# Optimization experiments

Hardware: AMD Instinct MI355X
Metric: run time of the kernel (lower is better)

The kernel has to match this reference:

```python
import jax, jax.numpy as jnp
import numpy as np
from jax import lax


def _conv_layer(x, K, k, stride, pad):
    """Faithful reimplementation of the custom Conv2d, including its two quirks:
    1) weight/input flatten-order mismatch: K.reshape(k*k*cin, cout) pairs flat
       index m (decoded as kh,kw,cin for K) against x flattened as (cin,kh,kw),
       so the effective conv weight is K.reshape(-1,cout).reshape(cin,k,k,cout).
    2) the python loop range(0, padd-k, stride) misses the last valid position
       whenever (padd-k) is divisible by stride, leaving last row/col zero.
    """
    B, cin, s_in, _ = x.shape
    cout = K.shape[-1]
    out_size = (s_in + 2 * pad - k) // stride + 1
    padd = s_in + 2 * pad
    n_loop = -(-(padd - k) // stride)  # = len(range(0, padd-k, stride))
    xp = jnp.pad(x, ((0, 0), (0, 0), (pad, pad), (pad, pad))) if pad > 0 else x
    # effective weight honoring the flatten-order mismatch: (cin, kh, kw, cout)
    W = K.reshape(-1, cout).reshape(cin, k, k, cout)
    y = lax.conv_general_dilated(
        xp, W, window_strides=(stride, stride), padding='VALID',
        dimension_numbers=('NCHW', 'IHWO', 'NCHW'))
    n = min(n_loop, out_size)
    out = jnp.zeros((B, cout, out_size, out_size), x.dtype)
    out = out.at[:, :, :n, :n].set(y[:, :, :n, :n])
    return out


def setup_inputs() -> dict:
    key = jax.random.key(0)
    ks = jax.random.split(key, 9)
    NUM_CLASSES = 10
    B = 8192

    def kinit(k_, shape):
        fan_in = shape[1] * int(np.prod(shape[2:]))  # torch fan_in for 4D
        bound = float(np.sqrt(6.0 / fan_in))
        return jax.random.uniform(k_, shape, jnp.float32, -bound, bound)

    x = jax.random.normal(ks[0], (B, 3, 28, 28), jnp.float32)
    K1 = kinit(ks[1], (5, 5, 3, 8))
    K2 = kinit(ks[2], (3, 3, 8, 16))
    K3 = kinit(ks[3], (3, 3, 16, 16))
    K4 = kinit(ks[4], (3, 3, 16, 16))
    K5 = kinit(ks[5], (3, 3, 16, 16))
    K6 = kinit(ks[6], (5, 5, 16, 32))
    fc_in = 6 * 6 * 32  # 1152
    bw = float(np.sqrt(1.0 / fc_in))
    Wfc = jax.random.uniform(ks[7], (NUM_CLASSES, fc_in), jnp.float32, -bw, bw)
    bfc = jax.random.uniform(ks[8], (NUM_CLASSES,), jnp.float32, -bw, bw)
    return {"x": x, "K1": K1, "K2": K2, "K3": K3, "K4": K4, "K5": K5,
            "K6": K6, "Wfc": Wfc, "bfc": bfc}


def reference(x, K1, K2, K3, K4, K5, K6, Wfc, bfc):
    h = jax.nn.relu(_conv_layer(x, K1, 5, 2, 1))   # (B,8,13,13)
    h = jax.nn.relu(_conv_layer(h, K2, 3, 1, 1))   # (B,16,13,13), last row/col zero
    h = jax.nn.relu(_conv_layer(h, K3, 3, 1, 1))
    h = jax.nn.relu(_conv_layer(h, K4, 3, 1, 1))
    h = jax.nn.relu(_conv_layer(h, K5, 3, 1, 1))
    h = _conv_layer(h, K6, 5, 2, 1)                # (B,32,6,6), last row/col zero
    flat = h.reshape(h.shape[0], -1)               # (B,1152)
    logits = flat @ Wfc.T + bfc
    return jax.nn.softmax(logits, axis=1)
```

## Files before the change

kernel.cpp:

```cpp
#include <hip/hip_runtime.h>
#include <hip/hip_bf16.h>
#include <math.h>

#define TPB 320

typedef __attribute__((ext_vector_type(8))) short short8;
typedef __attribute__((ext_vector_type(4))) float f32x4;
typedef unsigned short u16;

__device__ __forceinline__ f32x4 MFMA(short8 a, short8 b, f32x4 c) {
    return __builtin_amdgcn_mfma_f32_16x16x32_bf16(a, b, c, 0, 0, 0);
}
__device__ __forceinline__ u16 f2bf(float f) {
    unsigned int u = __builtin_bit_cast(unsigned int, f);
    u += 0x7FFFu + ((u >> 16) & 1u);
    return (u16)(u >> 16);
}
__device__ __forceinline__ u16 f2bf_hw(float f) {
    __hip_bfloat16 b = __float2bfloat16(f);
    return __builtin_bit_cast(u16, b);
}
__device__ __forceinline__ float bf2f(u16 h) {
    unsigned int u = ((unsigned int)h) << 16;
    return __builtin_bit_cast(float, u);
}

extern "C" __global__ void prep_w(const float* __restrict__ K1, const float* __restrict__ K2,
                                  const float* __restrict__ K3, const float* __restrict__ K4,
                                  const float* __restrict__ K5, const float* __restrict__ K6,
                                  short8* __restrict__ W)
{
    const int slot = blockIdx.x * blockDim.x + threadIdx.x;
    if (slot >= 6144) return;
    const int lane = slot & 63;
    const int ent  = slot >> 6;
    const int o    = lane & 15;
    const int lhi  = lane >> 4;
    float w[8];
    int hl;
    if (ent < 6) {
        const int s = ent >> 1; hl = ent & 1;
        const int t = s * 4 + lhi;
#pragma unroll
        for (int j = 0; j < 8; j++)
            w[j] = (t < 9) ? K2[(j * 9 + t) * 16 + o] : 0.f;
    } else if (ent < 36) {
        const int e  = ent - 6;
        const float* Kg = (e < 10) ? K3 : (e < 20) ? K4 : K5;
        const int el = e % 10;
        const int s  = el >> 1; hl = el & 1;
        const int chalf = (lhi & 1) * 8;
        const int t = 2 * s + (lhi >> 1);
#pragma unroll
        for (int j = 0; j < 8; j++)
            w[j] = (t < 9) ? Kg[((chalf + j) * 9 + t) * 16 + o] : 0.f;
    } else if (ent < 88) {
        const int e = ent - 36;
        const int s = e >> 2; hl = (e >> 1) & 1;
        const int nh = e & 1;
        const int chalf = (lhi & 1) * 8;
        const int t  = 2 * s + (lhi >> 1);
        const int oo = nh * 16 + o;
#pragma unroll
        for (int j = 0; j < 8; j++)
            w[j] = (t < 25) ? K6[((chalf + j) * 25 + t) * 32 + oo] : 0.f;
    } else {
        const int e = ent - 88;
        const int s = e >> 1; hl = e & 1;
        const int g  = s * 4 + lhi;
        const int gc = g > 14 ? 14 : g;
        const int c  = (gc * 52) >> 8;
        const int kh = gc - 5 * c;
#pragma unroll
        for (int j = 0; j < 8; j++)
            w[j] = (g < 15 && o < 8 && j < 5) ? K1[(c * 25 + kh * 5 + j) * 8 + o] : 0.f;
    }
    short8 v;
#pragma unroll
    for (int j = 0; j < 8; j++) {
        const u16 h = f2bf(w[j]);
        v[j] = hl ? (short)f2bf(w[j] - bf2f(h)) : (short)h;
    }
    W[slot] = v;
}


__device__ __forceinline__ void conv8(const u16* __restrict__ s0,
                                      u16* __restrict__ d0,
                                      const short8* __restrict__ Wt,
                                      int wave, int lane, int rot)
{
    const int o   = lane & 15;
    const int lhi = lane >> 4;
    short8 Bhi[3], Blo[3];
#pragma unroll
    for (int s = 0; s < 3; s++) {
        Bhi[s] = Wt[(s * 2 + 0) * 64 + lane];
        Blo[s] = Wt[(s * 2 + 1) * 64 + lane];
    }
    const u16* sl = s0 + 3600;
    const int r0 = lane & 15;

    auto tile = [&](int m) {
        const int p  = m * 16 + r0;
        const int ip = (p * 683) >> 13;
        const int jp = p - 12 * ip;
        f32x4 acc = {0.f, 0.f, 0.f, 0.f};
#pragma unroll
        for (int s = 0; s < 3; s++) {
            const int t  = s * 4 + lhi;
            const int tt = t > 8 ? 8 : t;
            const int kh = (tt * 11) >> 5;
            const int kw = tt - 3 * kh;
            const int px = (ip + kh) * 15 + (jp + kw);
            const short8 Ahi = *(const short8*)(s0 + px * 8);
            const short8 Alo = *(const short8*)(sl + px * 8);
            acc = MFMA(Ahi, Bhi[s], acc);
            acc = MFMA(Alo, Bhi[s], acc);
            acc = MFMA(Ahi, Blo[s], acc);
        }
        const int p0 = m * 16 + lhi * 4;
#pragma unroll
        for (int r = 0; r < 4; r++) {
            const int pp = p0 + r;
            const int ii = (pp * 683) >> 13;
            const int jj = pp - 12 * ii;
            const float v = fmaxf(acc[r], 0.f);
            const u16 h = f2bf_hw(v);
            const int px2 = (ii + 1) * 15 + (jj + 1);
            const int da  = (o >> 3) * 1800 + px2 * 8 + (o & 7);
            d0[da]        = h;
            d0[da + 3600] = f2bf_hw(v - bf2f(h));
        }
    };
    int m0 = wave + rot;
    if (m0 >= 5) m0 -= 5;
    tile(m0);
    if (m0 <= 3) tile(m0 + 5);
}

__device__ __forceinline__ void conv16(const u16* __restrict__ s0,
                                       u16* __restrict__ d0,
                                       const short8* __restrict__ Wt,
                                       int wave, int lane, int rot)
{
    const int o    = lane & 15;
    const int lhi  = lane >> 4;
    const int hsel = lhi & 1;
    const int tsel = lhi >> 1;
    short8 Bhi[5], Blo[5];
#pragma unroll
    for (int s = 0; s < 5; s++) {
        Bhi[s] = Wt[(s * 2 + 0) * 64 + lane];
        Blo[s] = Wt[(s * 2 + 1) * 64 + lane];
    }
    const u16* sh = s0 + hsel * 1800;
    const u16* sl = sh + 3600;
    const int r0 = lane & 15;

    auto tile = [&](int m) {
        const int p  = m * 16 + r0;
        const int ip = (p * 683) >> 13;
        const int jp = p - 12 * ip;
        f32x4 acc = {0.f, 0.f, 0.f, 0.f};
#pragma unroll
        for (int s = 0; s < 5; s++) {
            const int t  = 2 * s + tsel;
            const int tt = t > 8 ? 8 : t;
            const int kh = (tt * 11) >> 5;
            const int kw = tt - 3 * kh;
            const int px = (ip + kh) * 15 + (jp + kw);
            const short8 Ahi = *(const short8*)(sh + px * 8);
            const short8 Alo = *(const short8*)(sl + px * 8);
            acc = MFMA(Ahi, Bhi[s], acc);
            acc = MFMA(Alo, Bhi[s], acc);
            acc = MFMA(Ahi, Blo[s], acc);
        }
        const int p0 = m * 16 + lhi * 4;
#pragma unroll
        for (int r = 0; r < 4; r++) {
            const int pp = p0 + r;
            const int ii = (pp * 683) >> 13;
            const int jj = pp - 12 * ii;
            const float v = fmaxf(acc[r], 0.f);
            const u16 h = f2bf_hw(v);
            const int px2 = (ii + 1) * 15 + (jj + 1);
            const int da  = (o >> 3) * 1800 + px2 * 8 + (o & 7);
            d0[da]        = h;
            d0[da + 3600] = f2bf_hw(v - bf2f(h));
        }
    };
    int m0 = wave + rot;
    if (m0 >= 5) m0 -= 5;
    tile(m0);
    if (m0 <= 3) tile(m0 + 5);
}

extern "C" __global__ void __launch_bounds__(TPB)
cnn_fused(const float* __restrict__ xg,
          const float* __restrict__ Wfc, const float* __restrict__ bfc,
          const short8* __restrict__ W, float* __restrict__ out)
{
    __shared__ __align__(16) unsigned char smem[28864];
    u16*   const Ah   = (u16*)smem;
    u16*   const Bh   = (u16*)(smem + 14400);
    u16*   const Sh   = (u16*)(smem + 14400);
    float* const sF   = (float*)(smem + 14400);
    float* const sLog = (float*)(smem + 28800);
    uint4* const z4   = (uint4*)smem;
    const uint4 Z = {0u, 0u, 0u, 0u};

    const int tid  = threadIdx.x;
    const int lane = tid & 63;
    const int wave = tid >> 6;
    const int img  = blockIdx.x;

    for (int i = tid; i < 1804; i += TPB) z4[i] = Z;
    __syncthreads();

    const float4* xi4 = (const float4*)(xg + (size_t)img * 2352);
    for (int i4 = tid; i4 < 588; i4 += TPB) {
        const float4 v = xi4[i4];
        const int c = i4 / 196;
        const int rem = i4 - c * 196;
        const int r = rem / 7;
        const int q = rem - r * 7;
        const int ad = c * 960 + (r + 1) * 32 + q * 4 + 1;
        const float vv[4] = {v.x, v.y, v.z, v.w};
#pragma unroll
        for (int e = 0; e < 4; e++) {
            const u16 h = f2bf_hw(vv[e]);
            Sh[ad + e]        = h;
            Sh[ad + e + 2880] = f2bf_hw(vv[e] - bf2f(h));
        }
    }
    __syncthreads();

    {
        const short8* Wt1 = W + 5632;
        const int o   = lane & 15;
        const int lhi = lane >> 4;
        short8 B1h[4], B1l[4];
#pragma unroll
        for (int s = 0; s < 4; s++) {
            B1h[s] = Wt1[(s * 2 + 0) * 64 + lane];
            B1l[s] = Wt1[(s * 2 + 1) * 64 + lane];
        }
        const u16* slo = Sh + 2880;
        for (int m = wave; m < 11; m += 5) {
            const int p  = m * 16 + o;
            const int pc = p > 168 ? 168 : p;
            const int i = (pc * 316) >> 12;
            const int j = pc - 13 * i;
            f32x4 acc = {0.f, 0.f, 0.f, 0.f};
#pragma unroll
            for (int s = 0; s < 4; s++) {
                const int g  = s * 4 + lhi;
                const int gc = g > 14 ? 14 : g;
                const int c  = (gc * 52) >> 8;
                const int kh = gc - 5 * c;
                const int ad = c * 960 + (2 * i + kh) * 32 + 2 * j;
                const short8 Ahi = *(const short8*)(Sh + ad);
                const short8 Alo = *(const short8*)(slo + ad);
                acc = MFMA(Ahi, B1h[s], acc);
                acc = MFMA(Alo, B1h[s], acc);
                acc = MFMA(Ahi, B1l[s], acc);
            }
#pragma unroll
            for (int r = 0; r < 4; r++) {
                const int pp = m * 16 + lhi * 4 + r;
                if (pp < 169 && o < 8) {
                    const int ii = (pp * 316) >> 12;
                    const int jj = pp - 13 * ii;
                    const float v = fmaxf(acc[r], 0.f);
                    const u16 h = f2bf_hw(v);
                    const int da = ((ii + 1) * 15 + (jj + 1)) * 8 + o;
                    Ah[da]        = h;
                    Ah[da + 3600] = f2bf_hw(v - bf2f(h));
                }
            }
        }
    }
    __syncthreads();

    conv8(Ah, Bh, W, wave, lane, 0);
    if (tid < 208) {
        const int pl = tid / 52, e = tid - pl * 52;
        const int px = (e < 14) ? e
                     : (e < 28) ? 195 + (e - 14)
                     : (e < 40) ? (e - 27) * 15
                                : (e - 39) * 15 + 13;
        z4[900 + pl * 225 + px] = Z;
    }
    __syncthreads();

    conv16(Bh, Ah, W + 384, wave, lane, 1);
    if (tid < 108) {
        const int pl = tid / 27, e = tid - pl * 27;
        const int px = (e < 14) ? 195 + e : (e - 14) * 15 + 13;
        z4[pl * 225 + px] = Z;
    }
    __syncthreads();

    conv16(Ah, Bh, W + 1024, wave, lane, 2);
    __syncthreads();
    conv16(Bh, Ah, W + 1664, wave, lane, 3);
    __syncthreads();

    for (int i = tid; i < 352; i += TPB) {
        const int o = i / 11, k = i - o * 11;
        const int slot = (k < 6) ? o * 36 + 30 + k : o * 36 + (k - 6) * 6 + 5;
        sF[slot] = 0.f;
    }
    if (wave < 4) {
        const short8* Wt6 = W + 2304;
        const int mt   = wave >> 1;
        const int nh   = wave & 1;
        const int lhi  = lane >> 4;
        const int hsel = lhi & 1;
        const int tsel = lhi >> 1;
        const int o    = nh * 16 + (lane & 15);
        const int pr = mt * 16 + (lane & 15);
        const int pe = pr < 25 ? pr : 0;
        const int ia = (pe * 52) >> 8;
        const int ja = pe - 5 * ia;
        const u16* sh = Ah + hsel * 1800;
        const u16* sl = sh + 3600;
        f32x4 acc = {0.f, 0.f, 0.f, 0.f};
#pragma unroll 4
        for (int s = 0; s < 13; s++) {
            const int t  = 2 * s + tsel;
            const int tt = t > 24 ? 24 : t;
            const int kh = (tt * 52) >> 8;
            const int kw = tt - 5 * kh;
            const int px = (2 * ia + kh) * 15 + (2 * ja + kw);
            const short8 Ahi = *(const short8*)(sh + px * 8);
            const short8 Alo = *(const short8*)(sl + px * 8);
            const short8 Bh2 = Wt6[((s * 2 + 0) * 2 + nh) * 64 + lane];
            const short8 Bl2 = Wt6[((s * 2 + 1) * 2 + nh) * 64 + lane];
            acc = MFMA(Ahi, Bh2, acc);
            acc = MFMA(Alo, Bh2, acc);
            acc = MFMA(Ahi, Bl2, acc);
        }
        const int p0 = mt * 16 + lhi * 4;
#pragma unroll
        for (int r = 0; r < 4; r++) {
            const int pp = p0 + r;
            if (pp < 25) {
                const int ii = (pp * 52) >> 8;
                const int jj = pp - 5 * ii;
                sF[o * 36 + ii * 6 + jj] = acc[r];
            }
        }
    }
    __syncthreads();

    if (tid < 160) {
        const int c = tid >> 4;
        const int l = tid & 15;
        const float4* fv = (const float4*)(sF + l * 72);
        const float4* wv = (const float4*)(Wfc + c * 1152 + l * 72);
        float p = 0.f;
#pragma unroll
        for (int m = 0; m < 18; m++) {
            const float4 a = fv[m];
            const float4 b = wv[m];
            p = fmaf(a.x, b.x, p);
            p = fmaf(a.y, b.y, p);
            p = fmaf(a.z, b.z, p);
            p = fmaf(a.w, b.w, p);
        }
        p += __shfl_down(p, 8, 16);
        p += __shfl_down(p, 4, 16);
        p += __shfl_down(p, 2, 16);
        p += __shfl_down(p, 1, 16);
        if (l == 0) sLog[c] = p + bfc[c];
    }
    __syncthreads();

    if (tid < 10) {
        float mx = sLog[0];
#pragma unroll
        for (int k = 1; k < 10; k++) mx = fmaxf(mx, sLog[k]);
        float s = 0.f;
#pragma unroll
        for (int k = 0; k < 10; k++) s += expf(sLog[k] - mx);
        out[(size_t)img * 10 + tid] = expf(sLog[tid] - mx) / s;
    }
}

extern "C" void kernel_launch(void* const* d_in, const int* in_sizes, int n_in,
                              void* d_out, int out_size, void* d_ws, size_t ws_size,
                              hipStream_t stream) {
    const float* x   = (const float*)d_in[0];
    const float* K1  = (const float*)d_in[1];
    const float* K2  = (const float*)d_in[2];
    const float* K3  = (const float*)d_in[3];
    const float* K4  = (const float*)d_in[4];
    const float* K5  = (const float*)d_in[5];
    const float* K6  = (const float*)d_in[6];
    const float* Wfc = (const float*)d_in[7];
    const float* bfc = (const float*)d_in[8];
    float* out = (float*)d_out;
    short8* W = (short8*)d_ws;

    prep_w<<<24, 256, 0, stream>>>(K1, K2, K3, K4, K5, K6, W);

    const int B = in_sizes[0] / 2352;
    cnn_fused<<<B, TPB, 0, stream>>>(x, Wfc, bfc, W, out);
}
```

Baseline: 251.9 us.

## Use four waves per block and split MFMA accumulators into two chains

Reduces the block from five to four waves and redistributes the 9 (or 11) M-tiles of each conv stage across four waves, with wave 0 taking an extra tile. Each MFMA sequence now accumulates into two independent accumulators (hi*hi vs correction terms), summed at the end, which shortens the dependent MFMA chain. Fewer threads per block could allow more resident blocks, but the work is less evenly balanced across waves and register use rises. Other stages that use tid thresholds (e.g. tid<208, tid<160) still fit within 256 threads.

```diff
diff --git a/kernel.cpp b/kernel.cpp
--- a/kernel.cpp
+++ b/kernel.cpp
@@ -2,7 +2,7 @@
 #include <hip/hip_bf16.h>
 #include <math.h>
 
-#define TPB 320
+#define TPB 256
 
 typedef __attribute__((ext_vector_type(8))) short short8;
 typedef __attribute__((ext_vector_type(4))) float f32x4;
@@ -105,7 +105,8 @@
         const int p  = m * 16 + r0;
         const int ip = (p * 683) >> 13;
         const int jp = p - 12 * ip;
-        f32x4 acc = {0.f, 0.f, 0.f, 0.f};
+        f32x4 accA = {0.f, 0.f, 0.f, 0.f};
+        f32x4 accB = {0.f, 0.f, 0.f, 0.f};
 #pragma unroll
         for (int s = 0; s < 3; s++) {
             const int t  = s * 4 + lhi;
@@ -115,9 +116,9 @@
             const int px = (ip + kh) * 15 + (jp + kw);
             const short8 Ahi = *(const short8*)(s0 + px * 8);
             const short8 Alo = *(const short8*)(sl + px * 8);
-            acc = MFMA(Ahi, Bhi[s], acc);
-            acc = MFMA(Alo, Bhi[s], acc);
-            acc = MFMA(Ahi, Blo[s], acc);
+            accA = MFMA(Ahi, Bhi[s], accA);
+            accB = MFMA(Alo, Bhi[s], accB);
+            accB = MFMA(Ahi, Blo[s], accB);
         }
         const int p0 = m * 16 + lhi * 4;
 #pragma unroll
@@ -125,7 +126,7 @@
             const int pp = p0 + r;
             const int ii = (pp * 683) >> 13;
             const int jj = pp - 12 * ii;
-            const float v = fmaxf(acc[r], 0.f);
+            const float v = fmaxf(accA[r] + accB[r], 0.f);
             const u16 h = f2bf_hw(v);
             const int px2 = (ii + 1) * 15 + (jj + 1);
             const int da  = (o >> 3) * 1800 + px2 * 8 + (o & 7);
@@ -133,10 +134,10 @@
             d0[da + 3600] = f2bf_hw(v - bf2f(h));
         }
     };
-    int m0 = wave + rot;
-    if (m0 >= 5) m0 -= 5;
+    const int m0 = (wave + rot) & 3;
     tile(m0);
-    if (m0 <= 3) tile(m0 + 5);
+    tile(m0 + 4);
+    if (m0 == 0) tile(8);
 }
 
 __device__ __forceinline__ void conv16(const u16* __restrict__ s0,
@@ -162,7 +163,8 @@
         const int p  = m * 16 + r0;
         const int ip = (p * 683) >> 13;
         const int jp = p - 12 * ip;
-        f32x4 acc = {0.f, 0.f, 0.f, 0.f};
+        f32x4 accA = {0.f, 0.f, 0.f, 0.f};
+        f32x4 accB = {0.f, 0.f, 0.f, 0.f};
 #pragma unroll
         for (int s = 0; s < 5; s++) {
             const int t  = 2 * s + tsel;
@@ -172,9 +174,9 @@
             const int px = (ip + kh) * 15 + (jp + kw);
             const short8 Ahi = *(const short8*)(sh + px * 8);
             const short8 Alo = *(const short8*)(sl + px * 8);
-            acc = MFMA(Ahi, Bhi[s], acc);
-            acc = MFMA(Alo, Bhi[s], acc);
-            acc = MFMA(Ahi, Blo[s], acc);
+            accA = MFMA(Ahi, Bhi[s], accA);
+            accB = MFMA(Alo, Bhi[s], accB);
+            accB = MFMA(Ahi, Blo[s], accB);
         }
         const int p0 = m * 16 + lhi * 4;
 #pragma unroll
@@ -182,7 +184,7 @@
             const int pp = p0 + r;
             const int ii = (pp * 683) >> 13;
             const int jj = pp - 12 * ii;
-            const float v = fmaxf(acc[r], 0.f);
+            const float v = fmaxf(accA[r] + accB[r], 0.f);
             const u16 h = f2bf_hw(v);
             const int px2 = (ii + 1) * 15 + (jj + 1);
             const int da  = (o >> 3) * 1800 + px2 * 8 + (o & 7);
@@ -190,10 +192,10 @@
             d0[da + 3600] = f2bf_hw(v - bf2f(h));
         }
     };
-    int m0 = wave + rot;
-    if (m0 >= 5) m0 -= 5;
+    const int m0 = (wave + rot) & 3;
     tile(m0);
-    if (m0 <= 3) tile(m0 + 5);
+    tile(m0 + 4);
+    if (m0 == 0) tile(8);
 }
 
 extern "C" __global__ void __launch_bounds__(TPB)
@@ -247,12 +249,13 @@
             B1l[s] = Wt1[(s * 2 + 1) * 64 + lane];
         }
         const u16* slo = Sh + 2880;
-        for (int m = wave; m < 11; m += 5) {
+        for (int m = wave; m < 11; m += 4) {
             const int p  = m * 16 + o;
             const int pc = p > 168 ? 168 : p;
             const int i = (pc * 316) >> 12;
             const int j = pc - 13 * i;
-            f32x4 acc = {0.f, 0.f, 0.f, 0.f};
+            f32x4 accA = {0.f, 0.f, 0.f, 0.f};
+            f32x4 accB = {0.f, 0.f, 0.f, 0.f};
 #pragma unroll
             for (int s = 0; s < 4; s++) {
                 const int g  = s * 4 + lhi;
@@ -262,9 +265,9 @@
                 const int ad = c * 960 + (2 * i + kh) * 32 + 2 * j;
                 const short8 Ahi = *(const short8*)(Sh + ad);
                 const short8 Alo = *(const short8*)(slo + ad);
-                acc = MFMA(Ahi, B1h[s], acc);
-                acc = MFMA(Alo, B1h[s], acc);
-                acc = MFMA(Ahi, B1l[s], acc);
+                accA = MFMA(Ahi, B1h[s], accA);
+                accB = MFMA(Alo, B1h[s], accB);
+                accB = MFMA(Ahi, B1l[s], accB);
             }
 #pragma unroll
             for (int r = 0; r < 4; r++) {
@@ -272,7 +275,7 @@
                 if (pp < 169 && o < 8) {
                     const int ii = (pp * 316) >> 12;
                     const int jj = pp - 13 * ii;
-                    const float v = fmaxf(acc[r], 0.f);
+                    const float v = fmaxf(accA[r] + accB[r], 0.f);
                     const u16 h = f2bf_hw(v);
                     const int da = ((ii + 1) * 15 + (jj + 1)) * 8 + o;
                     Ah[da]        = h;
@@ -326,7 +329,8 @@
         const int ja = pe - 5 * ia;
         const u16* sh = Ah + hsel * 1800;
         const u16* sl = sh + 3600;
-        f32x4 acc = {0.f, 0.f, 0.f, 0.f};
+        f32x4 accA = {0.f, 0.f, 0.f, 0.f};
+        f32x4 accB = {0.f, 0.f, 0.f, 0.f};
 #pragma unroll 4
         for (int s = 0; s < 13; s++) {
             const int t  = 2 * s + tsel;
@@ -338,9 +342,9 @@
             const short8 Alo = *(const short8*)(sl + px * 8);
             const short8 Bh2 = Wt6[((s * 2 + 0) * 2 + nh) * 64 + lane];
             const short8 Bl2 = Wt6[((s * 2 + 1) * 2 + nh) * 64 + lane];
-            acc = MFMA(Ahi, Bh2, acc);
-            acc = MFMA(Alo, Bh2, acc);
-            acc = MFMA(Ahi, Bl2, acc);
+            accA = MFMA(Ahi, Bh2, accA);
+            accB = MFMA(Alo, Bh2, accB);
+            accB = MFMA(Ahi, Bl2, accB);
         }
         const int p0 = mt * 16 + lhi * 4;
 #pragma unroll
@@ -349,7 +353,7 @@
             if (pp < 25) {
                 const int ii = (pp * 52) >> 8;
                 const int jj = pp - 5 * ii;
-                sF[o * 36 + ii * 6 + jj] = acc[r];
+                sF[o * 36 + ii * 6 + jj] = accA[r] + accB[r];
             }
         }
     }
```

Result: faster. 232.1 us (-7.8%).
